# Optimization experiments

Hardware: AMD Instinct MI355X
Metric: run time of the kernel (lower is better)

Reference implementation:

```python
import jax, jax.numpy as jnp
import numpy as np

TEMPERATURE = 0.07
SIM_THRESHOLD = 0.5


def setup_inputs() -> dict:
    key = jax.random.key(0)
    k1, k2 = jax.random.split(key)
    features = jax.random.normal(k1, (4096, 2, 128), dtype=jnp.float32)
    labels = jax.random.randint(k2, (4096, 100), 0, 2).astype(jnp.float32)
    return {"features": features, "labels": labels}


def reference(features, labels):
    B, V, D = features.shape

    # label Jaccard similarity -> positive/negative masks [B, B]
    intersection = labels @ labels.T
    row_sum = jnp.sum(labels, axis=1, keepdims=True)
    union = row_sum + row_sum.T - intersection
    similarity = intersection / (union + 1e-6)
    positive_mask = (similarity >= SIM_THRESHOLD).astype(jnp.float32)
    negative_mask = 1.0 - positive_mask

    # torch.cat(torch.unbind(features, dim=1), dim=0) -> [V*B, D] (view-major)
    contrast_feature = jnp.transpose(features, (1, 0, 2)).reshape(V * B, D)
    dot_similarities = (contrast_feature @ contrast_feature.T) / TEMPERATURE  # [VB, VB]

    # numerical stability: subtract detached row max over the FULL row
    logits_max = jax.lax.stop_gradient(jnp.max(dot_similarities, axis=1, keepdims=True))
    logits = dot_similarities - logits_max

    # only the top-left [B, B] block is ever indexed by the original loop
    e = jnp.exp(logits[:B, :B])
    pos_sum = jnp.sum(e * positive_mask, axis=1)  # [B]
    neg_sum = jnp.sum(e * negative_mask, axis=1)  # [B]

    has_pos = jnp.sum(positive_mask, axis=1) > 0  # rows with >=1 positive
    pos_safe = jnp.where(has_pos, pos_sum, 1.0)
    den_safe = jnp.where(has_pos, pos_sum + neg_sum, 1.0)
    per_row = -jnp.log(pos_safe / den_safe)

    count = jnp.sum(has_pos.astype(jnp.float32))
    loss = jnp.sum(jnp.where(has_pos, per_row, 0.0)) / jnp.maximum(count, 1.0)
    return loss
```

## Files before the change

### kernel.cpp

```cpp
#include <hip/hip_runtime.h>
#include <math.h>

#define B_ROWS 4096
#define LBL 100
#define NCT 32
#define NTRI 528

typedef __attribute__((ext_vector_type(8))) short bf16x8;
typedef __attribute__((ext_vector_type(4))) float f32x4;

__device__ __forceinline__ unsigned f2bf(float x) {
  union { float f; unsigned u; } a; a.f = x;
  unsigned r = a.u + 0x7fffu + ((a.u >> 16) & 1u);
  return r >> 16;
}
__device__ __forceinline__ float bf2f(unsigned h) {
  return __uint_as_float(h << 16);
}

__global__ void prep_kernel(const float* __restrict__ feat,
                            const float* __restrict__ labels,
                            uint4* __restrict__ cf,
                            uint4* __restrict__ Lb,
                            int* __restrict__ rsv,
                            float* __restrict__ seedRaw,
                            float* __restrict__ accum,
                            unsigned* __restrict__ counter) {
  if (blockIdx.x == 0 && threadIdx.x < 2) accum[threadIdx.x] = 0.0f;
  if (blockIdx.x == 0 && threadIdx.x == 2) *counter = 0u;
  int w = blockIdx.x * 4 + (threadIdx.x >> 6);
  int lane = threadIdx.x & 63;
  float2 f = ((const float2*)(feat + (size_t)w * 256))[lane];
  unsigned u0 = f2bf(f.x), u1 = f2bf(f.y);
  unsigned myu = u0 | (u1 << 16);
  float b0 = bf2f(u0), b1 = bf2f(u1);
  float s = b0 * b0 + b1 * b1;
  #pragma unroll
  for (int o = 32; o >= 1; o >>= 1) s += __shfl_xor(s, o);
  float x0 = labels[(size_t)w * LBL + lane];
  float x1 = (lane < LBL - 64) ? labels[(size_t)w * LBL + 64 + lane] : 0.0f;
  unsigned long long m0 = __ballot(x0 != 0.0f);
  unsigned long long m1 = __ballot(x1 != 0.0f);
  int kc = lane & 15;
  unsigned q0 = __shfl(myu, kc * 4 + 0);
  unsigned q1 = __shfl(myu, kc * 4 + 1);
  unsigned q2 = __shfl(myu, kc * 4 + 2);
  unsigned q3 = __shfl(myu, kc * 4 + 3);
  if (lane < 16)
    cf[(size_t)(w >> 7) * 2048 + kc * 128 + ((w & 127) ^ kc)] =
        make_uint4(q0, q1, q2, q3);
  if (lane == 0) {
    Lb[w] = make_uint4((unsigned)m0, (unsigned)(m0 >> 32),
                       (unsigned)m1, (unsigned)(m1 >> 32));
    rsv[w] = __popcll(m0) + __popcll(m1);
    seedRaw[w] = s - 0.15f;
  }
}

__launch_bounds__(256)
__global__ void main_kernel(const uint4* __restrict__ cf,
                            const uint4* __restrict__ Lb,
                            const int* __restrict__ rsv,
                            const float* __restrict__ seedRaw,
                            float2* __restrict__ part2) {
  int bid = blockIdx.x;
  int bx = 0, off = 0;
  while (bid >= off + (NCT - bx)) { off += NCT - bx; ++bx; }
  int by = bx + (bid - off);
  const bool diag = (bx == by);

  const int tid = threadIdx.x;
  const int lane = tid & 63;
  const int l15 = lane & 15;
  const int quad = lane >> 4;
  const int wave = tid >> 6;
  const int wi = (wave & 1) * 64;
  const int wj = (wave >> 1) * 64;
  const int rowBase = bx * 128;
  const int colBase = by * 128;
  const float invT = 1.0f / 0.07f;

  const uint4* Ab = cf + (size_t)bx * 2048;
  const uint4* Bb = cf + (size_t)by * 2048;

  f32x4 acc[4][4];
  #pragma unroll
  for (int ti = 0; ti < 4; ++ti)
    #pragma unroll
    for (int tj = 0; tj < 4; ++tj)
      acc[ti][tj] = (f32x4){0.f, 0.f, 0.f, 0.f};

  bf16x8 af[4], bfr[4], af2[4], bfr2[4];
  {
    const int kc = quad;
    #pragma unroll
    for (int t = 0; t < 4; ++t) {
      af[t]  = *(const bf16x8*)&Ab[kc * 128 + ((wi + t * 16 + l15) ^ kc)];
      bfr[t] = *(const bf16x8*)&Bb[kc * 128 + ((wj + t * 16 + l15) ^ kc)];
    }
  }
  #pragma unroll
  for (int ks = 0; ks < 4; ++ks) {
    if (ks < 3) {
      const int kc = (ks + 1) * 4 + quad;
      #pragma unroll
      for (int t = 0; t < 4; ++t) {
        af2[t]  = *(const bf16x8*)&Ab[kc * 128 + ((wi + t * 16 + l15) ^ kc)];
        bfr2[t] = *(const bf16x8*)&Bb[kc * 128 + ((wj + t * 16 + l15) ^ kc)];
      }
    }
    #pragma unroll
    for (int ti = 0; ti < 4; ++ti)
      #pragma unroll
      for (int tj = 0; tj < 4; ++tj)
        acc[ti][tj] = __builtin_amdgcn_mfma_f32_16x16x32_bf16(
            af[ti], bfr[tj], acc[ti][tj], 0, 0, 0);
    if (ks < 3) {
      #pragma unroll
      for (int t = 0; t < 4; ++t) { af[t] = af2[t]; bfr[t] = bfr2[t]; }
    }
  }

  uint4 clb[4];
  int crs[4];
  float scol[4], srow[16];
  #pragma unroll
  for (int tj = 0; tj < 4; ++tj) {
    int gcol = colBase + wj + tj * 16 + l15;
    clb[tj] = Lb[gcol];
    crs[tj] = rsv[gcol];
    scol[tj] = seedRaw[gcol];
  }
  #pragma unroll
  for (int ti = 0; ti < 4; ++ti) {
    float4 s4 = *(const float4*)&seedRaw[rowBase + wi + ti * 16 + quad * 4];
    srow[ti * 4 + 0] = s4.x; srow[ti * 4 + 1] = s4.y;
    srow[ti * 4 + 2] = s4.z; srow[ti * 4 + 3] = s4.w;
  }

  float p_s[16], n_s[16], cp[4], cn[4], cmax[4];
  #pragma unroll
  for (int i = 0; i < 16; ++i) { p_s[i] = 0.f; n_s[i] = 0.f; }
  #pragma unroll
  for (int tj = 0; tj < 4; ++tj) { cp[tj] = 0.f; cn[tj] = 0.f; cmax[tj] = -1e30f; }

  #pragma unroll
  for (int ti = 0; ti < 4; ++ti)
    #pragma unroll
    for (int r = 0; r < 4; ++r) {
      int si = ti * 4 + r;
      float l0 = acc[ti][0][r], l1 = acc[ti][1][r];
      float l2 = acc[ti][2][r], l3 = acc[ti][3][r];
      cmax[0] = fmaxf(cmax[0], l0);
      cmax[1] = fmaxf(cmax[1], l1);
      cmax[2] = fmaxf(cmax[2], l2);
      cmax[3] = fmaxf(cmax[3], l3);
      float tm = fmaxf(fmaxf(l0, l1), fmaxf(l2, l3));
      if (tm > srow[si] - 6.3f) {
        int grow = rowBase + wi + ti * 16 + quad * 4 + r;
        uint4 la = Lb[grow];
        int ra = rsv[grow];
        float p = p_s[si], n = n_s[si];
        float lv[4] = {l0, l1, l2, l3};
        #pragma unroll
        for (int tj = 0; tj < 4; ++tj) {
          float e = __expf((lv[tj] - srow[si]) * invT);
          int inter = __popc(la.x & clb[tj].x) + __popc(la.y & clb[tj].y) +
                      __popc(la.z & clb[tj].z) + __popc(la.w & clb[tj].w);
          if (3 * inter > ra + crs[tj]) p += e; else n += e;
        }
        p_s[si] = p;
        n_s[si] = n;
      }
    }

  if (!diag) {
    #pragma unroll
    for (int tj = 0; tj < 4; ++tj) {
      if (cmax[tj] > scol[tj] - 6.3f) {
        float p = cp[tj], n = cn[tj];
        #pragma unroll
        for (int ti = 0; ti < 4; ++ti)
          #pragma unroll
          for (int r = 0; r < 4; ++r) {
            float e = __expf((acc[ti][tj][r] - scol[tj]) * invT);
            int grow = rowBase + wi + ti * 16 + quad * 4 + r;
            uint4 la = Lb[grow];
            int inter = __popc(la.x & clb[tj].x) + __popc(la.y & clb[tj].y) +
                        __popc(la.z & clb[tj].z) + __popc(la.w & clb[tj].w);
            if (3 * inter > rsv[grow] + crs[tj]) p += e; else n += e;
          }
        cp[tj] = p;
        cn[tj] = n;
      }
    }
  }

  #pragma unroll
  for (int si = 0; si < 16; ++si) {
    float p = p_s[si], n = n_s[si];
    #pragma unroll
    for (int o = 8; o >= 1; o >>= 1) {
      p += __shfl_xor(p, o);
      n += __shfl_xor(n, o);
    }
    p_s[si] = p;
    n_s[si] = n;
  }
  if (l15 == 0) {
    int sc = by * 2 + (wj >> 6);
    #pragma unroll
    for (int ti = 0; ti < 4; ++ti)
      #pragma unroll
      for (int r = 0; r < 4; ++r) {
        int row = rowBase + wi + ti * 16 + quad * 4 + r;
        part2[(size_t)sc * B_ROWS + row] =
            make_float2(p_s[ti * 4 + r], n_s[ti * 4 + r]);
      }
  }
  #pragma unroll
  for (int tj = 0; tj < 4; ++tj) {
    float p = cp[tj], n = cn[tj];
    p += __shfl_xor(p, 16); n += __shfl_xor(n, 16);
    p += __shfl_xor(p, 32); n += __shfl_xor(n, 32);
    cp[tj] = p;
    cn[tj] = n;
  }
  if (!diag && quad == 0) {
    int sc = bx * 2 + (wi >> 6);
    #pragma unroll
    for (int tj = 0; tj < 4; ++tj) {
      int col = colBase + wj + tj * 16 + l15;
      part2[(size_t)sc * B_ROWS + col] = make_float2(cp[tj], cn[tj]);
    }
  }
}

__global__ void mergefin_kernel(const float2* __restrict__ part2,
                                const int* __restrict__ rsv,
                                float* __restrict__ accum,
                                unsigned* __restrict__ counter,
                                float* __restrict__ out) {
  int row = blockIdx.x * 256 + threadIdx.x;
  float p = 0.f, n = 0.f;
  #pragma unroll
  for (int c = 0; c < 2 * NCT; ++c) {
    float2 v = part2[(size_t)c * B_ROWS + row];
    p += v.x;
    n += v.y;
  }
  float per = 0.f, cnt = 0.f;
  if (rsv[row] > 0) {
    per = -logf(p / (p + n));
    cnt = 1.f;
  }
  #pragma unroll
  for (int o = 32; o >= 1; o >>= 1) {
    per += __shfl_xor(per, o);
    cnt += __shfl_xor(cnt, o);
  }
  if ((threadIdx.x & 63) == 0) {
    atomicAdd(accum + 0, per);
    atomicAdd(accum + 1, cnt);
  }
  __syncthreads();
  __threadfence();
  __shared__ unsigned done;
  if (threadIdx.x == 0) done = atomicAdd(counter, 1u);
  __syncthreads();
  if (done == 15 && threadIdx.x == 0) {
    __threadfence();
    float P = atomicAdd(accum + 0, 0.0f);
    float C = atomicAdd(accum + 1, 0.0f);
    out[0] = P / fmaxf(C, 1.0f);
  }
}

extern "C" void kernel_launch(void* const* d_in, const int* in_sizes, int n_in,
                              void* d_out, int out_size, void* d_ws, size_t ws_size,
                              hipStream_t stream) {
  const float* feat = (const float*)d_in[0];
  const float* labels = (const float*)d_in[1];
  float* out = (float*)d_out;
  char* ws = (char*)d_ws;
  uint4* cf = (uint4*)(ws + 0);
  uint4* Lbm = (uint4*)(ws + 1048576);
  int* rsv = (int*)(ws + 1114112);
  float* seedRaw = (float*)(ws + 1130496);
  float2* part2 = (float2*)(ws + 1146880);
  float* accum = (float*)(ws + 1146880 + 2097152);
  unsigned* counter = (unsigned*)(ws + 1146880 + 2097152 + 8);

  hipLaunchKernelGGL(prep_kernel, dim3(1024), dim3(256), 0, stream,
                     feat, labels, cf, Lbm, rsv, seedRaw, accum, counter);
  hipLaunchKernelGGL(main_kernel, dim3(NTRI), dim3(256), 0, stream,
                     cf, Lbm, rsv, seedRaw, part2);
  hipLaunchKernelGGL(mergefin_kernel, dim3(B_ROWS / 256), dim3(256), 0, stream,
                     part2, rsv, accum, counter, out);
}
```

Before: 83.02 us.

## Fuse row reduction into main kernel via atomics and last-block finalize

Drops the separate merge kernel and its partial-sum buffer. Main-kernel blocks now atomically add row and column positive/negative sums into a per-row accumulator, skipping zero contributions. The last block to finish, detected with a global counter, computes the per-row log terms and writes the loss. This removes one kernel launch and the write and re-read of the partial buffer. In exchange it adds float atomic traffic and contention, makes the summation order nondeterministic, and leaves the final reduction to a single block.

```diff
diff --git a/kernel.cpp b/kernel.cpp
--- a/kernel.cpp
+++ b/kernel.cpp
@@ -24,10 +24,9 @@
                             uint4* __restrict__ Lb,
                             int* __restrict__ rsv,
                             float* __restrict__ seedRaw,
-                            float* __restrict__ accum,
+                            float2* __restrict__ rowAcc,
                             unsigned* __restrict__ counter) {
-  if (blockIdx.x == 0 && threadIdx.x < 2) accum[threadIdx.x] = 0.0f;
-  if (blockIdx.x == 0 && threadIdx.x == 2) *counter = 0u;
+  if (blockIdx.x == 0 && threadIdx.x == 0) *counter = 0u;
   int w = blockIdx.x * 4 + (threadIdx.x >> 6);
   int lane = threadIdx.x & 63;
   float2 f = ((const float2*)(feat + (size_t)w * 256))[lane];
@@ -54,6 +53,7 @@
                        (unsigned)m1, (unsigned)(m1 >> 32));
     rsv[w] = __popcll(m0) + __popcll(m1);
     seedRaw[w] = s - 0.15f;
+    rowAcc[w] = make_float2(0.0f, 0.0f);
   }
 }
 
@@ -62,7 +62,12 @@
                             const uint4* __restrict__ Lb,
                             const int* __restrict__ rsv,
                             const float* __restrict__ seedRaw,
-                            float2* __restrict__ part2) {
+                            float2* __restrict__ rowAcc,
+                            unsigned* __restrict__ counter,
+                            float* __restrict__ out) {
+  __shared__ unsigned s_done;
+  __shared__ float s_p[4], s_c[4];
+
   int bid = blockIdx.x;
   int bx = 0, off = 0;
   while (bid >= off + (NCT - bx)) { off += NCT - bx; ++bx; }
@@ -208,14 +213,16 @@
     n_s[si] = n;
   }
   if (l15 == 0) {
-    int sc = by * 2 + (wj >> 6);
     #pragma unroll
     for (int ti = 0; ti < 4; ++ti)
       #pragma unroll
       for (int r = 0; r < 4; ++r) {
-        int row = rowBase + wi + ti * 16 + quad * 4 + r;
-        part2[(size_t)sc * B_ROWS + row] =
-            make_float2(p_s[ti * 4 + r], n_s[ti * 4 + r]);
+        float p = p_s[ti * 4 + r], n = n_s[ti * 4 + r];
+        if (p != 0.f || n != 0.f) {
+          int row = rowBase + wi + ti * 16 + quad * 4 + r;
+          atomicAdd(&rowAcc[row].x, p);
+          atomicAdd(&rowAcc[row].y, n);
+        }
       }
   }
   #pragma unroll
@@ -227,52 +234,47 @@
     cn[tj] = n;
   }
   if (!diag && quad == 0) {
-    int sc = bx * 2 + (wi >> 6);
     #pragma unroll
     for (int tj = 0; tj < 4; ++tj) {
-      int col = colBase + wj + tj * 16 + l15;
-      part2[(size_t)sc * B_ROWS + col] = make_float2(cp[tj], cn[tj]);
-    }
-  }
-}
-
-__global__ void mergefin_kernel(const float2* __restrict__ part2,
-                                const int* __restrict__ rsv,
-                                float* __restrict__ accum,
-                                unsigned* __restrict__ counter,
-                                float* __restrict__ out) {
-  int row = blockIdx.x * 256 + threadIdx.x;
-  float p = 0.f, n = 0.f;
-  #pragma unroll
-  for (int c = 0; c < 2 * NCT; ++c) {
-    float2 v = part2[(size_t)c * B_ROWS + row];
-    p += v.x;
-    n += v.y;
-  }
-  float per = 0.f, cnt = 0.f;
-  if (rsv[row] > 0) {
-    per = -logf(p / (p + n));
-    cnt = 1.f;
-  }
-  #pragma unroll
-  for (int o = 32; o >= 1; o >>= 1) {
-    per += __shfl_xor(per, o);
-    cnt += __shfl_xor(cnt, o);
-  }
-  if ((threadIdx.x & 63) == 0) {
-    atomicAdd(accum + 0, per);
-    atomicAdd(accum + 1, cnt);
-  }
+      if (cp[tj] != 0.f || cn[tj] != 0.f) {
+        int col = colBase + wj + tj * 16 + l15;
+        atomicAdd(&rowAcc[col].x, cp[tj]);
+        atomicAdd(&rowAcc[col].y, cn[tj]);
+      }
+    }
+  }
+
+  __threadfence();
+  if (tid == 0) s_done = atomicAdd(counter, 1u);
   __syncthreads();
-  __threadfence();
-  __shared__ unsigned done;
-  if (threadIdx.x == 0) done = atomicAdd(counter, 1u);
-  __syncthreads();
-  if (done == 15 && threadIdx.x == 0) {
+  if (s_done == NTRI - 1) {
     __threadfence();
-    float P = atomicAdd(accum + 0, 0.0f);
-    float C = atomicAdd(accum + 1, 0.0f);
-    out[0] = P / fmaxf(C, 1.0f);
+    float per = 0.f, cnt = 0.f;
+    #pragma unroll
+    for (int it = 0; it < B_ROWS / 256; ++it) {
+      int row = it * 256 + tid;
+      unsigned long long u = __hip_atomic_load(
+          (const unsigned long long*)&rowAcc[row], __ATOMIC_RELAXED,
+          __HIP_MEMORY_SCOPE_AGENT);
+      float p = __uint_as_float((unsigned)u);
+      float n = __uint_as_float((unsigned)(u >> 32));
+      if (rsv[row] > 0) {
+        per += -logf(p / (p + n));
+        cnt += 1.f;
+      }
+    }
+    #pragma unroll
+    for (int o = 32; o >= 1; o >>= 1) {
+      per += __shfl_xor(per, o);
+      cnt += __shfl_xor(cnt, o);
+    }
+    if ((tid & 63) == 0) { s_p[tid >> 6] = per; s_c[tid >> 6] = cnt; }
+    __syncthreads();
+    if (tid == 0) {
+      float P = s_p[0] + s_p[1] + s_p[2] + s_p[3];
+      float C = s_c[0] + s_c[1] + s_c[2] + s_c[3];
+      out[0] = P / fmaxf(C, 1.0f);
+    }
   }
 }
 
@@ -287,14 +289,11 @@
   uint4* Lbm = (uint4*)(ws + 1048576);
   int* rsv = (int*)(ws + 1114112);
   float* seedRaw = (float*)(ws + 1130496);
-  float2* part2 = (float2*)(ws + 1146880);
-  float* accum = (float*)(ws + 1146880 + 2097152);
-  unsigned* counter = (unsigned*)(ws + 1146880 + 2097152 + 8);
+  float2* rowAcc = (float2*)(ws + 1146880);
+  unsigned* counter = (unsigned*)(ws + 1146880 + 32768);
 
   hipLaunchKernelGGL(prep_kernel, dim3(1024), dim3(256), 0, stream,
-                     feat, labels, cf, Lbm, rsv, seedRaw, accum, counter);
+                     feat, labels, cf, Lbm, rsv, seedRaw, rowAcc, counter);
   hipLaunchKernelGGL(main_kernel, dim3(NTRI), dim3(256), 0, stream,
-                     cf, Lbm, rsv, seedRaw, part2);
-  hipLaunchKernelGGL(mergefin_kernel, dim3(B_ROWS / 256), dim3(256), 0, stream,
-                     part2, rsv, accum, counter, out);
-}
+                     cf, Lbm, rsv, seedRaw, rowAcc, counter, out);
+}
```

Result: slower. 108.3 us (+30.5%).
